# Optimization experiments

Hardware: AMD Instinct MI355X
Metric: run time of the kernel (lower is better)

## Reference

```python
import jax, jax.numpy as jnp
import numpy as np

B, T, F = 8, 1024, 80
STACK, STRIDE = 4, 4          # encoder.embed.right_context+1, subsampling_rate
G, E, C = 4, 16, 8192         # num_codebooks, embedding_dim, num_embeddings
DENC = 512                    # encoder.output_size()
TS = (T - STACK) // STRIDE + 1
FREG = 0.01                   # features_regularization_weight
EPS = 1e-5


def setup_inputs() -> dict:
    key = jax.random.key(0)
    ks = jax.random.split(key, 12)
    feats = jax.random.normal(ks[0], (B, T, F), jnp.float32)
    feats_lengths = jax.random.randint(ks[1], (B,), T // 2, T + 1, jnp.int32)
    # span masks (True = masked), mask_length=10 spans so full subsample windows get masked
    n_spans, ML = 16, 10
    starts = jax.random.randint(ks[2], (B, n_spans), 0, T - ML)
    pos = starts[:, :, None] + jnp.arange(ML)  # [B, n_spans, ML]
    masks = jnp.zeros((B, T), bool).at[jnp.arange(B)[:, None, None], pos].set(True)
    mask_emb = 0.1 * jax.random.normal(ks[3], (1, 1, F), jnp.float32)
    signal_mean = 0.1 * jax.random.normal(ks[4], (F,), jnp.float32)
    signal_istd = jax.random.uniform(ks[5], (F,), jnp.float32, 0.5, 1.5)
    projection = jax.random.normal(ks[6], (STACK * F, G * E), jnp.float32) * np.sqrt(2.0 / (STACK * F + G * E))
    embeddings = jax.random.normal(ks[7], (C, G, E), jnp.float32)
    encoder_top_n_out = 0.02 * jax.random.normal(ks[8], (G, DENC, C), jnp.float32)
    encoder_top_n_out_bias = jnp.zeros((G, C), jnp.float32)
    encoder_out = jax.random.normal(ks[9], (B, TS, DENC), jnp.float32)
    return {"feats": feats, "feats_lengths": feats_lengths, "masks": masks,
            "mask_emb": mask_emb, "signal_mean": signal_mean, "signal_istd": signal_istd,
            "projection": projection, "embeddings": embeddings,
            "encoder_top_n_out": encoder_top_n_out,
            "encoder_top_n_out_bias": encoder_top_n_out_bias,
            "encoder_out": encoder_out}


def _quantize_codes(latent, codebook):
    # latent: [N, G*E] -> codes [N, G]; codebook: [C, G, E]
    lat = latent.reshape(latent.shape[0], G, E)
    dist = (jnp.sum(lat ** 2, -1, keepdims=True)
            - 2.0 * jnp.einsum('ngd,cgd->ngc', lat, codebook)
            + jnp.sum(codebook ** 2, -1).T[None])  # [N, G, C]
    return jnp.argmin(dist, axis=-1)


def reference(feats, feats_lengths, masks, mask_emb, signal_mean, signal_istd,
              projection, embeddings, encoder_top_n_out, encoder_top_n_out_bias,
              encoder_out):
    # global CMVN
    xs = (feats - signal_mean) * signal_istd  # [B, T, F]
    features_pen = jnp.mean(xs ** 2)
    # masked signal (fed to the delegated encoder in the original; encoder_out stands in)
    _masked_xs = jnp.where(masks[:, :, None], mask_emb, xs)
    # unfold windows
    widx = jnp.arange(TS)[:, None] * STRIDE + jnp.arange(STACK)  # [TS, STACK]
    code_ids_mask = jnp.all(masks[:, widx], axis=2)  # [B, TS] (torch.min over bool window)
    stacked = xs[:, widx].reshape(B, TS, STACK * F)  # _stack_features on unmasked input
    # LayerNorm (no affine)
    mu = jnp.mean(stacked, -1, keepdims=True)
    var = jnp.var(stacked, -1, keepdims=True)
    normed = (stacked - mu) / jnp.sqrt(var + EPS)
    proj = normed @ projection  # [B, TS, G*E]
    target = _quantize_codes(proj.reshape(B * TS, G * E), embeddings).reshape(B, TS, G)
    # encoder output mask after subsampling
    lens_sub = jnp.maximum((feats_lengths - STACK) // STRIDE + 1, 0)
    out_mask = jnp.arange(TS)[None, :] < lens_sub[:, None]
    m = (out_mask & code_ids_mask).astype(jnp.float32)  # [B, TS]
    # big matmul: [B,1,TS,DENC] x [1,G,DENC,C] + bias -> [B,G,TS,C]
    logits = jnp.einsum('btd,gdc->bgtc', encoder_out, encoder_top_n_out) \
             + encoder_top_n_out_bias[None, :, None, :]
    logp = jax.nn.log_softmax(logits, axis=-1).transpose(0, 2, 1, 3)  # [B, TS, G, C]
    per = -jnp.take_along_axis(logp, target[..., None], axis=-1)[..., 0]  # [B, TS, G]
    denom = jnp.sum(m) + 1e-5
    loss = jnp.sum(per * m[:, :, None]) / (denom * G) + FREG * features_pen
    num_codes = jnp.sum(m) * G
    corr = (jnp.argmax(logits, -1).transpose(0, 2, 1) == target)
    codes_acc = jnp.sum(corr * m[:, :, None]) / num_codes
    vals = (target * m[:, :, None].astype(target.dtype)).reshape(-1)
    uniq_num_codes = jnp.zeros((C,), bool).at[vals].set(True).sum()
    return (loss, codes_acc, features_pen, num_codes, uniq_num_codes)
```

## Files before the change

kernel.cpp:

```cpp
#include <hip/hip_runtime.h>
#include <hip/hip_bf16.h>
#include <math.h>
#include <stddef.h>

#define NB 8
#define NT 1024
#define NF 80
#define NSTACK 4
#define NSTRIDE 4
#define NG 4
#define NE 16
#define NC 8192
#define ND 512
#define NTS 256
#define NP (NB*NTS)
#define SFD (NSTACK*NF)
#define FREG 0.01f
#define LNEPS 1e-5f

#define TCC 1024
#define CPT 4
#define PCH 16
#define PB 16

#define ROWS_MAX 2176
#define ROWCH 144
#define MT 9
#define QCH 16
#define QY 16
#define CT 128
#define QS 8

typedef __attribute__((ext_vector_type(8))) short short8;
typedef __attribute__((ext_vector_type(4))) float f32x4;

struct Ws {
  float penSum;
  unsigned int nA;
  unsigned int maskIsInt;
  unsigned int pad1;
  unsigned long long amax[NP*NG];
  float sumExp[NP*NG];
  float tLogit[NP*NG];
  int   targets[NP*NG];
  int   activeList[NP];
  unsigned int bitmap[NC/32];
  unsigned long long aminS[NP*NG*QS];
  float lat[NP][64];
  unsigned short aHiT[(size_t)(ND/8)*ROWS_MAX*8];
  unsigned short aLoT[(size_t)(ND/8)*ROWS_MAX*8];
  float part_se[NG][ROWS_MAX][CT];
  unsigned long long part_mx[NG][ROWS_MAX][CT];
};

__device__ inline unsigned short bf16_rne(float x) {
  unsigned u = __float_as_uint(x);
  unsigned r = u + 0x7FFFu + ((u >> 16) & 1u);
  return (unsigned short)(r >> 16);
}
__device__ inline unsigned fkey_asc(float d) {
  unsigned u = __float_as_uint(d);
  return (u & 0x80000000u) ? ~u : (u | 0x80000000u);
}

__global__ __launch_bounds__(256) void k_prologue(
    const float* __restrict__ feats, const float* __restrict__ mean,
    const float* __restrict__ istd, const unsigned char* __restrict__ m8,
    const int* __restrict__ lens, int doClear, Ws* ws) {
  const int tid = threadIdx.x;
  if (doClear) ws->aminS[(size_t)blockIdx.x*256 + tid] = ~0ull;

  const int N4 = NB*NT*NF/4;
  float s = 0.f;
  for (int i = blockIdx.x*256 + tid; i < N4; i += gridDim.x*256) {
    float4 v = reinterpret_cast<const float4*>(feats)[i];
    int f0 = (i*4) % NF;
    float x0 = (v.x - mean[f0+0]) * istd[f0+0];
    float x1 = (v.y - mean[f0+1]) * istd[f0+1];
    float x2 = (v.z - mean[f0+2]) * istd[f0+2];
    float x3 = (v.w - mean[f0+3]) * istd[f0+3];
    s += x0*x0 + x1*x1 + x2*x2 + x3*x3;
  }
  for (int o = 32; o; o >>= 1) s += __shfl_down(s, o);
  __shared__ float pr[4];
  if ((tid & 63) == 0) pr[tid >> 6] = s;
  __syncthreads();
  if (tid == 0) atomicAdd(&ws->penSum, pr[0]+pr[1]+pr[2]+pr[3]);

  if (blockIdx.x < NP/256) {
    __shared__ unsigned flag;
    if (tid == 0) flag = 0;
    __syncthreads();
    unsigned nz = 0;
    int base = tid * 32;
    for (int i = base; i < base + 32; ++i)
      if ((i & 3) && m8[i]) nz = 1;
    if (nz) atomicOr(&flag, 1u);
    __syncthreads();
    bool isInt = (flag == 0);

    int p = blockIdx.x*256 + tid;
    int b = p >> 8, ts = p & (NTS-1);
    int t0 = b*NT + ts*NSTRIDE;
    bool allm;
    if (isInt) {
      const int* m32 = (const int*)m8;
      allm = m32[t0] && m32[t0+1] && m32[t0+2] && m32[t0+3];
    } else {
      allm = m8[t0] && m8[t0+1] && m8[t0+2] && m8[t0+3];
    }
    int ls = (lens[b] - NSTACK)/NSTRIDE + 1;
    if (ls < 0) ls = 0;
    if (allm && ts < ls) {
      unsigned idx = atomicAdd(&ws->nA, 1u);
      ws->activeList[idx] = p;
    }
  }
}

__global__ __launch_bounds__(256) void k_latprep(
    const float* __restrict__ feats, const float* __restrict__ mean,
    const float* __restrict__ istd, const float* __restrict__ projw,
    const float* __restrict__ enc, Ws* ws) {
  int nA = (int)ws->nA;
  int ai = blockIdx.x;
  int limit = ((nA + ROWCH - 1) / ROWCH) * ROWCH;
  int tid = threadIdx.x;

  if (ai >= nA) {
    if (ai < limit && tid < 64) {
      short8 z;
      #pragma unroll
      for (int j = 0; j < 8; ++j) z[j] = 0;
      *reinterpret_cast<short8*>(ws->aHiT + ((size_t)tid*ROWS_MAX + ai)*8) = z;
      *reinterpret_cast<short8*>(ws->aLoT + ((size_t)tid*ROWS_MAX + ai)*8) = z;
    }
    return;
  }

  int p = ws->activeList[ai];
  if (tid < 64) {
    const float* src = enc + (size_t)p*ND + tid*8;
    float4 x0 = *reinterpret_cast<const float4*>(src);
    float4 x1 = *reinterpret_cast<const float4*>(src + 4);
    float xv[8] = {x0.x, x0.y, x0.z, x0.w, x1.x, x1.y, x1.z, x1.w};
    short8 h, l;
    #pragma unroll
    for (int j = 0; j < 8; ++j) {
      unsigned short hi = bf16_rne(xv[j]);
      float rem = xv[j] - __uint_as_float((unsigned)hi << 16);
      h[j] = (short)hi;
      l[j] = (short)bf16_rne(rem);
    }
    *reinterpret_cast<short8*>(ws->aHiT + ((size_t)tid*ROWS_MAX + ai)*8) = h;
    *reinterpret_cast<short8*>(ws->aLoT + ((size_t)tid*ROWS_MAX + ai)*8) = l;
  }

  int b = p >> 8, ts = p & (NTS-1);
  __shared__ float sN[SFD];
  __shared__ float sPart[4*64];
  __shared__ float rS[4], rQ[4];

  for (int j = tid; j < SFD; j += 256) {
    int k = j / NF, f = j - k*NF;
    sN[j] = (feats[((size_t)b*NT + ts*NSTRIDE + k)*NF + f] - mean[f]) * istd[f];
  }
  __syncthreads();
  float s = 0.f, q = 0.f;
  for (int j = tid; j < SFD; j += 256) { float x = sN[j]; s += x; q += x*x; }
  for (int o = 32; o; o >>= 1) { s += __shfl_down(s, o); q += __shfl_down(q, o); }
  if ((tid & 63) == 0) { rS[tid>>6] = s; rQ[tid>>6] = q; }
  __syncthreads();
  float mu  = (rS[0]+rS[1]+rS[2]+rS[3]) * (1.f/SFD);
  float var = (rQ[0]+rQ[1]+rQ[2]+rQ[3]) * (1.f/SFD) - mu*mu;
  float inv = rsqrtf(var + LNEPS);
  for (int j = tid; j < SFD; j += 256) sN[j] = (sN[j]-mu)*inv;
  __syncthreads();
  {
    int j = tid & 63, part = tid >> 6;
    float a = 0.f;
    int i0 = part*80;
    for (int i = i0; i < i0+80; ++i) a = fmaf(sN[i], projw[i*64 + j], a);
    sPart[part*64 + j] = a;
  }
  __syncthreads();
  if (tid < 64)
    ws->lat[ai][tid] = sPart[tid] + sPart[64+tid] + sPart[128+tid] + sPart[192+tid];
}

__global__ __launch_bounds__(256) void k_qdist(const float* __restrict__ emb, Ws* ws) {
  int nA = (int)ws->nA;
  if (nA == 0) return;
  int tid = threadIdx.x;
  int g = tid >> 6, lane = tid & 63;
  int c = blockIdx.x * 64 + lane;
  int per = (nA + QY - 1) / QY;
  int a0 = blockIdx.y * per;
  int a1 = min(nA, a0 + per);
  int slot = blockIdx.x & (QS-1);

  const float4* e4 = reinterpret_cast<const float4*>(emb + ((size_t)c*NG + g)*NE);
  float4 b0 = e4[0], b1 = e4[1], b2 = e4[2], b3 = e4[3];
  float n2 = b0.x*b0.x + b0.y*b0.y + b0.z*b0.z + b0.w*b0.w
           + b1.x*b1.x + b1.y*b1.y + b1.z*b1.z + b1.w*b1.w
           + b2.x*b2.x + b2.y*b2.y + b2.z*b2.z + b2.w*b2.w
           + b3.x*b3.x + b3.y*b3.y + b3.z*b3.z + b3.w*b3.w;

  __shared__ float sL[QCH][64];
  for (int base = a0; base < a1; base += QCH) {
    int cnt = min(QCH, a1 - base);
    __syncthreads();
    for (int i = tid; i < cnt*64; i += 256)
      (&sL[0][0])[i] = (&ws->lat[0][0])[(size_t)(base + (i >> 6))*64 + (i & 63)];
    __syncthreads();
    for (int i = 0; i < cnt; ++i) {
      const float* lp = &sL[i][g*NE];
      float dot = lp[0]*b0.x + lp[1]*b0.y + lp[2]*b0.z + lp[3]*b0.w
                + lp[4]*b1.x + lp[5]*b1.y + lp[6]*b1.z + lp[7]*b1.w
                + lp[8]*b2.x + lp[9]*b2.y + lp[10]*b2.z + lp[11]*b2.w
                + lp[12]*b3.x + lp[13]*b3.y + lp[14]*b3.z + lp[15]*b3.w;
      float d = n2 - 2.f*dot;
      float mv = d; int mc = c;
      #pragma unroll
      for (int off = 32; off; off >>= 1) {
        float ov = __shfl_xor(mv, off);
        int   oc = __shfl_xor(mc, off);
        if (ov < mv || (ov == mv && oc < mc)) { mv = ov; mc = oc; }
      }
      if (lane == 0) {
        unsigned long long key =
            ((unsigned long long)fkey_asc(mv) << 32) | (unsigned)mc;
        atomicMin(&ws->aminS[(size_t)((base + i)*NG + g)*QS + slot], key);
      }
    }
  }
}

__global__ void k_tgt(Ws* ws) {
  int i = blockIdx.x*256 + threadIdx.x;
  int nA = (int)ws->nA;
  if (i < nA*NG) {
    unsigned long long m = ws->aminS[(size_t)i*QS];
    #pragma unroll
    for (int s = 1; s < QS; ++s) {
      unsigned long long v = ws->aminS[(size_t)i*QS + s];
      if (v < m) m = v;
    }
    int c = (int)(unsigned)(m & 0xFFFFFFFFull);
    ws->targets[i] = c;
    atomicOr(&ws->bitmap[c >> 5], 1u << (c & 31));
  }
}

__global__ __launch_bounds__(512, 4) void k_logits_mfma(
    const float* __restrict__ W, const float* __restrict__ bias, Ws* ws) {
  const int nA = (int)ws->nA;
  if (nA == 0) return;
  const int nCh = (nA + ROWCH - 1) / ROWCH;
  const int tid = threadIdx.x;
  const int wave = tid >> 6, lane = tid & 63;
  const int sub = wave & 3, kh = wave >> 2;
  const int g = blockIdx.y;
  const int c0w = blockIdx.x * 64 + sub * 16;
  const int lo16 = lane & 15, hi4 = lane >> 4;
  const int cA = c0w + lo16;
  const int cOut0 = c0w + hi4*4;
  float bv[4];
  #pragma unroll
  for (int v = 0; v < 4; ++v) bv[v] = bias[g*NC + cOut0 + v];

  __shared__ f32x4 sAcc[4][MT][64];
  __shared__ float sEs[4][ROWCH];
  __shared__ unsigned long long sMx[4][ROWCH];

  for (int ch = 0; ch < nCh; ++ch) {
    const int r0 = ch * ROWCH;
    f32x4 acc[MT];
    #pragma unroll
    for (int mt = 0; mt < MT; ++mt) acc[mt] = (f32x4){0.f, 0.f, 0.f, 0.f};

    for (int ks = kh*8; ks < kh*8 + 8; ++ks) {
      short8 bh[MT], bl[MT];
      const size_t boff = ((size_t)(ks*4 + hi4)*ROWS_MAX + r0 + lo16)*8;
      #pragma unroll
      for (int mt = 0; mt < MT; ++mt) {
        bh[mt] = *reinterpret_cast<const short8*>(ws->aHiT + boff + (size_t)mt*128);
        bl[mt] = *reinterpret_cast<const short8*>(ws->aLoT + boff + (size_t)mt*128);
      }
      const float* wp = W + ((size_t)g*ND + ks*32 + hi4*8)*NC + cA;
      float wv[8];
      #pragma unroll
      for (int j = 0; j < 8; ++j) wv[j] = wp[(size_t)j*NC];
      short8 whi, wlo;
      #pragma unroll
      for (int j = 0; j < 8; ++j) {
        unsigned short h = bf16_rne(wv[j]);
        float rem = wv[j] - __uint_as_float((unsigned)h << 16);
        whi[j] = (short)h;
        wlo[j] = (short)bf16_rne(rem);
      }
      #pragma unroll
      for (int mt = 0; mt < MT; ++mt) {
        acc[mt] = __builtin_amdgcn_mfma_f32_16x16x32_bf16(whi, bh[mt], acc[mt], 0, 0, 0);
        acc[mt] = __builtin_amdgcn_mfma_f32_16x16x32_bf16(wlo, bh[mt], acc[mt], 0, 0, 0);
        acc[mt] = __builtin_amdgcn_mfma_f32_16x16x32_bf16(whi, bl[mt], acc[mt], 0, 0, 0);
      }
    }

    if (kh == 1) {
      #pragma unroll
      for (int mt = 0; mt < MT; ++mt) sAcc[sub][mt][lane] = acc[mt];
    }
    __syncthreads();

    if (kh == 0) {
      #pragma unroll
      for (int mt = 0; mt < MT; ++mt) {
        f32x4 oth = sAcc[sub][mt][lane];
        const int row = r0 + mt*16 + lo16;
        const int tgt = (row < nA) ? ws->targets[row*NG + g] : -1;
        float lv[4];
        #pragma unroll
        for (int v = 0; v < 4; ++v) lv[v] = (acc[mt][v] + oth[v]) + bv[v];
        #pragma unroll
        for (int v = 0; v < 4; ++v)
          if (tgt == cOut0 + v) ws->tLogit[row*NG + g] = lv[v];
        float es = expf(lv[0]) + expf(lv[1]) + expf(lv[2]) + expf(lv[3]);
        float mv = lv[0]; int mi = cOut0;
        if (lv[1] > mv) { mv = lv[1]; mi = cOut0+1; }
        if (lv[2] > mv) { mv = lv[2]; mi = cOut0+2; }
        if (lv[3] > mv) { mv = lv[3]; mi = cOut0+3; }
        #pragma unroll
        for (int off = 16; off <= 32; off <<= 1) {
          es += __shfl_xor(es, off);
          float ov = __shfl_xor(mv, off);
          int   oi = __shfl_xor(mi, off);
          if (ov > mv || (ov == mv && oi < mi)) { mv = ov; mi = oi; }
        }
        if (hi4 == 0) {
          sEs[sub][mt*16 + lo16] = es;
          unsigned key = __float_as_uint(mv);
          key = (key & 0x80000000u) ? ~key : (key | 0x80000000u);
          sMx[sub][mt*16 + lo16] = ((unsigned long long)key << 32)
                                 | (unsigned long long)(0xFFFFFFFFu - (unsigned)mi);
        }
      }
    }
    __syncthreads();
    if (tid < ROWCH) {
      float e = sEs[0][tid] + sEs[1][tid] + sEs[2][tid] + sEs[3][tid];
      unsigned long long m0 = sMx[0][tid], m1 = sMx[1][tid];
      unsigned long long m2 = sMx[2][tid], m3 = sMx[3][tid];
      unsigned long long ma = m0 > m1 ? m0 : m1;
      unsigned long long mb = m2 > m3 ? m2 : m3;
      unsigned long long mx = ma > mb ? ma : mb;
      int grow = r0 + tid;
      ws->part_se[g][grow][blockIdx.x] = e;
      ws->part_mx[g][grow][blockIdx.x] = mx;
    }
    __syncthreads();
  }
}

__global__ __launch_bounds__(256) void k_red_l(Ws* ws) {
  int nA = (int)ws->nA;
  int pair = blockIdx.x*4 + (threadIdx.x >> 6);
  int lane = threadIdx.x & 63;
  int row = pair >> 2, g = pair & 3;
  if (row >= nA) return;
  float e = ws->part_se[g][row][lane] + ws->part_se[g][row][lane + 64];
  unsigned long long a = ws->part_mx[g][row][lane];
  unsigned long long b = ws->part_mx[g][row][lane + 64];
  unsigned long long mx = a > b ? a : b;
  #pragma unroll
  for (int off = 32; off; off >>= 1) {
    e += __shfl_xor(e, off);
    unsigned long long o = __shfl_xor(mx, off);
    if (o > mx) mx = o;
  }
  if (lane == 0) {
    ws->sumExp[row*NG + g] = e;
    ws->amax[row*NG + g] = mx;
  }
}

__global__ __launch_bounds__(256) void k_quant(
    const float* __restrict__ feats, const float* __restrict__ mean,
    const float* __restrict__ istd, const float* __restrict__ projw,
    const float* __restrict__ emb, Ws* ws) {
  if (blockIdx.x >= ws->nA) return;
  int ai = blockIdx.x;
  int p = ws->activeList[ai];
  int b = p >> 8, ts = p & (NTS-1);
  int tid = threadIdx.x;
  __shared__ float sN[SFD];
  __shared__ float sPart[4*64];
  __shared__ float sLat[NG*NE];
  __shared__ float sRedS[256];
  __shared__ int   sRedC[256];
  __shared__ float rS[4], rQ[4];
  __shared__ int   sTgt[NG];

  for (int j = tid; j < SFD; j += 256) {
    int k = j / NF, f = j - k*NF;
    sN[j] = (feats[((size_t)b*NT + ts*NSTRIDE + k)*NF + f] - mean[f]) * istd[f];
  }
  __syncthreads();
  float s = 0.f, q = 0.f;
  for (int j = tid; j < SFD; j += 256) { float x = sN[j]; s += x; q += x*x; }
  for (int o = 32; o; o >>= 1) { s += __shfl_down(s, o); q += __shfl_down(q, o); }
  if ((tid & 63) == 0) { rS[tid>>6] = s; rQ[tid>>6] = q; }
  __syncthreads();
  float mu  = (rS[0]+rS[1]+rS[2]+rS[3]) * (1.f/SFD);
  float var = (rQ[0]+rQ[1]+rQ[2]+rQ[3]) * (1.f/SFD) - mu*mu;
  float inv = rsqrtf(var + LNEPS);
  for (int j = tid; j < SFD; j += 256) sN[j] = (sN[j]-mu)*inv;
  __syncthreads();
  {
    int j = tid & 63, part = tid >> 6;
    float a = 0.f;
    int i0 = part*80;
    for (int i = i0; i < i0+80; ++i) a = fmaf(sN[i], projw[i*64 + j], a);
    sPart[part*64 + j] = a;
  }
  __syncthreads();
  if (tid < 64) sLat[tid] = sPart[tid] + sPart[64+tid] + sPart[128+tid] + sPart[192+tid];
  __syncthreads();

  for (int gg = 0; gg < NG; ++gg) {
    float lg[NE];
    #pragma unroll
    for (int e = 0; e < NE; ++e) lg[e] = sLat[gg*NE + e];
    float best = 3.4e38f; int bc = NC;
    for (int c = tid; c < NC; c += 256) {
      const float4* cb4 = reinterpret_cast<const float4*>(emb + ((size_t)c*NG + gg)*NE);
      float4 a0 = cb4[0], a1 = cb4[1], a2 = cb4[2], a3 = cb4[3];
      float dot = 0.f, n2 = 0.f;
      dot = fmaf(lg[0],  a0.x, dot); n2 = fmaf(a0.x, a0.x, n2);
      dot = fmaf(lg[1],  a0.y, dot); n2 = fmaf(a0.y, a0.y, n2);
      dot = fmaf(lg[2],  a0.z, dot); n2 = fmaf(a0.z, a0.z, n2);
      dot = fmaf(lg[3],  a0.w, dot); n2 = fmaf(a0.w, a0.w, n2);
      dot = fmaf(lg[4],  a1.x, dot); n2 = fmaf(a1.x, a1.x, n2);
      dot = fmaf(lg[5],  a1.y, dot); n2 = fmaf(a1.y, a1.y, n2);
      dot = fmaf(lg[6],  a1.z, dot); n2 = fmaf(a1.z, a1.z, n2);
      dot = fmaf(lg[7],  a1.w, dot); n2 = fmaf(a1.w, a1.w, n2);
      dot = fmaf(lg[8],  a2.x, dot); n2 = fmaf(a2.x, a2.x, n2);
      dot = fmaf(lg[9],  a2.y, dot); n2 = fmaf(a2.y, a2.y, n2);
      dot = fmaf(lg[10], a2.z, dot); n2 = fmaf(a2.z, a2.z, n2);
      dot = fmaf(lg[11], a2.w, dot); n2 = fmaf(a2.w, a2.w, n2);
      dot = fmaf(lg[12], a3.x, dot); n2 = fmaf(a3.x, a3.x, n2);
      dot = fmaf(lg[13], a3.y, dot); n2 = fmaf(a3.y, a3.y, n2);
      dot = fmaf(lg[14], a3.z, dot); n2 = fmaf(a3.z, a3.z, n2);
      dot = fmaf(lg[15], a3.w, dot); n2 = fmaf(a3.w, a3.w, n2);
      float sc = n2 - 2.f*dot;
      if (sc < best) { best = sc; bc = c; }
    }
    sRedS[tid] = best; sRedC[tid] = bc;
    __syncthreads();
    for (int off = 128; off; off >>= 1) {
      if (tid < off) {
        float os = sRedS[tid+off]; int oc = sRedC[tid+off];
        if (os < sRedS[tid] || (os == sRedS[tid] && oc < sRedC[tid])) {
          sRedS[tid] = os; sRedC[tid] = oc;
        }
      }
      __syncthreads();
    }
    if (tid == 0) sTgt[gg] = sRedC[0];
    __syncthreads();
  }
  if (tid < NG) {
    int c = sTgt[tid];
    ws->targets[ai*NG + tid] = c;
    atomicOr(&ws->bitmap[c >> 5], 1u << (c & 31));
  }
}

__global__ __launch_bounds__(256) void k_logits(
    const float* __restrict__ W, const float* __restrict__ bias,
    const float* __restrict__ enc, Ws* ws) {
  const int nA = (int)ws->nA;
  if (nA == 0) return;
  const int nCh = (nA + PCH - 1) / PCH;
  const int g = blockIdx.y;
  const int cbase = blockIdx.x * TCC + threadIdx.x * CPT;
  const float* __restrict__ Wg = W + (size_t)g*ND*NC;
  const float b0 = bias[g*NC + cbase + 0];
  const float b1 = bias[g*NC + cbase + 1];
  const float b2 = bias[g*NC + cbase + 2];
  const float b3 = bias[g*NC + cbase + 3];
  __shared__ float4 sEnc[PCH][ND/4];
  __shared__ int sP[PCH];

  for (int ch = blockIdx.z; ch < nCh; ch += PB) {
    if (threadIdx.x < PCH) {
      int ai = ch*PCH + threadIdx.x;
      sP[threadIdx.x] = (ai < nA) ? ws->activeList[ai] : -1;
    }
    __syncthreads();
    for (int i = threadIdx.x; i < PCH*(ND/4); i += 256) {
      int qq = i >> 7, r = i & 127;
      int p = sP[qq];
      sEnc[qq][r] = (p >= 0) ? reinterpret_cast<const float4*>(enc)[p*(ND/4) + r]
                             : make_float4(0.f, 0.f, 0.f, 0.f);
    }
    __syncthreads();

    float acc[PCH][CPT];
    #pragma unroll
    for (int qq = 0; qq < PCH; ++qq)
      #pragma unroll
      for (int j = 0; j < CPT; ++j) acc[qq][j] = 0.f;
    for (int d = 0; d < ND; d += 4) {
      const float* wp = Wg + (size_t)d*NC + cbase;
      float4 w0 = *reinterpret_cast<const float4*>(wp);
      float4 w1 = *reinterpret_cast<const float4*>(wp + NC);
      float4 w2 = *reinterpret_cast<const float4*>(wp + 2*NC);
      float4 w3 = *reinterpret_cast<const float4*>(wp + 3*NC);
      int dq = d >> 2;
      #pragma unroll
      for (int qq = 0; qq < PCH; ++qq) {
        float4 e = sEnc[qq][dq];
        acc[qq][0] = fmaf(e.x, w0.x, acc[qq][0]);
        acc[qq][1] = fmaf(e.x, w0.y, acc[qq][1]);
        acc[qq][2] = fmaf(e.x, w0.z, acc[qq][2]);
        acc[qq][3] = fmaf(e.x, w0.w, acc[qq][3]);
        acc[qq][0] = fmaf(e.y, w1.x, acc[qq][0]);
        acc[qq][1] = fmaf(e.y, w1.y, acc[qq][1]);
        acc[qq][2] = fmaf(e.y, w1.z, acc[qq][2]);
        acc[qq][3] = fmaf(e.y, w1.w, acc[qq][3]);
        acc[qq][0] = fmaf(e.z, w2.x, acc[qq][0]);
        acc[qq][1] = fmaf(e.z, w2.y, acc[qq][1]);
        acc[qq][2] = fmaf(e.z, w2.z, acc[qq][2]);
        acc[qq][3] = fmaf(e.z, w2.w, acc[qq][3]);
        acc[qq][0] = fmaf(e.w, w3.x, acc[qq][0]);
        acc[qq][1] = fmaf(e.w, w3.y, acc[qq][1]);
        acc[qq][2] = fmaf(e.w, w3.z, acc[qq][2]);
        acc[qq][3] = fmaf(e.w, w3.w, acc[qq][3]);
      }
    }

    #pragma unroll
    for (int qq = 0; qq < PCH; ++qq) {
      int ai = ch*PCH + qq;
      if (ai < nA) {
        float l0 = acc[qq][0] + b0;
        float l1 = acc[qq][1] + b1;
        float l2 = acc[qq][2] + b2;
        float l3 = acc[qq][3] + b3;
        int tgt = ws->targets[ai*NG + g];
        if ((unsigned)(tgt - cbase) < (unsigned)CPT) {
          float tv = (tgt == cbase) ? l0 : (tgt == cbase+1) ? l1
                   : (tgt == cbase+2) ? l2 : l3;
          ws->tLogit[ai*NG + g] = tv;
        }
        float es = expf(l0) + expf(l1) + expf(l2) + expf(l3);
        float mv = l0; int mi = cbase;
        if (l1 > mv) { mv = l1; mi = cbase+1; }
        if (l2 > mv) { mv = l2; mi = cbase+2; }
        if (l3 > mv) { mv = l3; mi = cbase+3; }
        for (int o = 32; o; o >>= 1) {
          es += __shfl_down(es, o);
          float ov = __shfl_down(mv, o);
          int   oi = __shfl_down(mi, o);
          if (ov > mv || (ov == mv && oi < mi)) { mv = ov; mi = oi; }
        }
        if ((threadIdx.x & 63) == 0) {
          atomicAdd(&ws->sumExp[ai*NG + g], es);
          unsigned key = __float_as_uint(mv);
          key = (key & 0x80000000u) ? ~key : (key | 0x80000000u);
          unsigned long long pk =
              ((unsigned long long)key << 32) |
              (unsigned long long)(0xFFFFFFFFu - (unsigned)mi);
          atomicMax(&ws->amax[ai*NG + g], pk);
        }
      }
    }
    __syncthreads();
  }
}

__global__ __launch_bounds__(256) void k_final(Ws* ws, float* __restrict__ out) {
  int tid = threadIdx.x;
  int nA = (int)ws->nA;
  float sumPer = 0.f, sumCorr = 0.f;
  for (int i = tid; i < nA*NG; i += 256) {
    sumPer += logf(ws->sumExp[i]) - ws->tLogit[i];
    unsigned long long pk = ws->amax[i];
    int mi = (int)(0xFFFFFFFFu - (unsigned)(pk & 0xFFFFFFFFull));
    if (mi == ws->targets[i]) sumCorr += 1.f;
  }
  unsigned w = ws->bitmap[tid];
  if (tid == 0 && nA < NP) w |= 1u;
  int uniq = __popc(w);

  __shared__ float rs[4], rc[4]; __shared__ int ru[4];
  float s1 = sumPer, s2 = sumCorr; int s3 = uniq;
  for (int o = 32; o; o >>= 1) {
    s1 += __shfl_down(s1, o);
    s2 += __shfl_down(s2, o);
    s3 += __shfl_down(s3, o);
  }
  if ((tid & 63) == 0) { rs[tid>>6] = s1; rc[tid>>6] = s2; ru[tid>>6] = s3; }
  __syncthreads();
  if (tid == 0) {
    float sp = rs[0]+rs[1]+rs[2]+rs[3];
    float sc = rc[0]+rc[1]+rc[2]+rc[3];
    int   un = ru[0]+ru[1]+ru[2]+ru[3];
    float pen   = ws->penSum / (float)(NB*NT*NF);
    float denom = (float)nA + 1e-5f;
    float nc    = (float)(nA * NG);
    out[0] = sp / (denom * (float)NG) + FREG * pen;
    out[1] = sc / nc;
    out[2] = pen;
    out[3] = nc;
    out[4] = (float)un;
  }
}

extern "C" void kernel_launch(void* const* d_in, const int* in_sizes, int n_in,
                              void* d_out, int out_size, void* d_ws, size_t ws_size,
                              hipStream_t stream) {
  const float* feats = (const float*)d_in[0];
  const int*   lens  = (const int*)d_in[1];
  const unsigned char* masks = (const unsigned char*)d_in[2];
  const float* mean  = (const float*)d_in[4];
  const float* istd  = (const float*)d_in[5];
  const float* projw = (const float*)d_in[6];
  const float* emb   = (const float*)d_in[7];
  const float* W     = (const float*)d_in[8];
  const float* bias  = (const float*)d_in[9];
  const float* enc   = (const float*)d_in[10];
  Ws* ws = (Ws*)d_ws;
  float* out = (float*)d_out;

  bool big = ws_size >= sizeof(Ws);
  size_t zr = offsetof(Ws, aminS);
  hipMemsetAsync(d_ws, 0, (big || ws_size >= zr) ? zr : ws_size, stream);

  k_prologue<<<256, 256, 0, stream>>>(feats, mean, istd, masks, lens,
                                      big ? 1 : 0, ws);

  if (big) {
    k_latprep<<<ROWS_MAX, 256, 0, stream>>>(feats, mean, istd, projw, enc, ws);
    k_qdist<<<dim3(NC/64, QY), 256, 0, stream>>>(emb, ws);
    k_tgt<<<NP*NG/256, 256, 0, stream>>>(ws);
    k_logits_mfma<<<dim3(CT, NG), 512, 0, stream>>>(W, bias, ws);
    k_red_l<<<NP, 256, 0, stream>>>(ws);
  } else {
    k_quant<<<NP, 256, 0, stream>>>(feats, mean, istd, projw, emb, ws);
    k_logits<<<dim3(NC/TCC, NG, PB), 256, 0, stream>>>(W, bias, enc, ws);
  }
  k_final<<<1, 256, 0, stream>>>(ws, out);
}
```

Baseline: 83.30 us.

## Stage activation tiles in LDS with double-buffered async loads in logits MFMA

The logits kernel drops the split-K wave arrangement, so all 8 waves now cover distinct 16-column slices (128 columns per block instead of 64). The bf16 hi/lo activation tiles are staged into shared memory with global_load_lds and double-buffered across the K steps, and W values are prefetched one step ahead. This is meant to let the waves share activation loads instead of each re-reading them from global memory, and to remove the cross-wave partial-accumulator reduction. In exchange it adds a barrier per K step and more LDS use, and it halves the column-tile count (CT 64), so the launch has fewer blocks and k_red_l reduces 64 partials instead of 128.

```diff
diff --git a/kernel.cpp b/kernel.cpp
--- a/kernel.cpp
+++ b/kernel.cpp
@@ -28,8 +28,9 @@
 #define MT 9
 #define QCH 16
 #define QY 16
-#define CT 128
+#define CT 64
 #define QS 8
+#define STG 1152
 
 typedef __attribute__((ext_vector_type(8))) short short8;
 typedef __attribute__((ext_vector_type(4))) float f32x4;
@@ -62,6 +63,11 @@
   unsigned u = __float_as_uint(d);
   return (u & 0x80000000u) ? ~u : (u | 0x80000000u);
 }
+__device__ __forceinline__ void gload_lds16(const void* g, void* l) {
+  __builtin_amdgcn_global_load_lds(
+      (const __attribute__((address_space(1))) void*)g,
+      (__attribute__((address_space(3))) void*)l, 16, 0, 0);
+}
 
 __global__ __launch_bounds__(256) void k_prologue(
     const float* __restrict__ feats, const float* __restrict__ mean,
@@ -259,9 +265,9 @@
   const int nCh = (nA + ROWCH - 1) / ROWCH;
   const int tid = threadIdx.x;
   const int wave = tid >> 6, lane = tid & 63;
-  const int sub = wave & 3, kh = wave >> 2;
+  const int sub = wave;
   const int g = blockIdx.y;
-  const int c0w = blockIdx.x * 64 + sub * 16;
+  const int c0w = blockIdx.x * 128 + sub * 16;
   const int lo16 = lane & 15, hi4 = lane >> 4;
   const int cA = c0w + lo16;
   const int cOut0 = c0w + hi4*4;
@@ -269,28 +275,62 @@
   #pragma unroll
   for (int v = 0; v < 4; ++v) bv[v] = bias[g*NC + cOut0 + v];
 
-  __shared__ f32x4 sAcc[4][MT][64];
-  __shared__ float sEs[4][ROWCH];
-  __shared__ unsigned long long sMx[4][ROWCH];
+  __shared__ unsigned short sB[2*STG*8];
+  __shared__ float sEs[8][ROWCH];
+  __shared__ unsigned long long sMx[8][ROWCH];
+
+  const unsigned short* gB[3];
+  #pragma unroll
+  for (int it = 0; it < 3; ++it) {
+    int t = tid + it*512;
+    if (t < STG) {
+      int hilo = t / 576;
+      int r = t - hilo*576;
+      int h4 = r / 144;
+      int row = r - h4*144;
+      gB[it] = (hilo ? ws->aLoT : ws->aHiT) + ((size_t)h4*ROWS_MAX + row)*8;
+    }
+  }
 
   for (int ch = 0; ch < nCh; ++ch) {
     const int r0 = ch * ROWCH;
+    const size_t chOff = (size_t)r0*8;
+
+    #pragma unroll
+    for (int it = 0; it < 3; ++it) {
+      int t = tid + it*512;
+      if (t < STG)
+        gload_lds16(gB[it] + chOff, sB + (size_t)t*8);
+    }
+    float wv[8];
+    {
+      const float* wp = W + ((size_t)g*ND + hi4*8)*NC + cA;
+      #pragma unroll
+      for (int j = 0; j < 8; ++j) wv[j] = wp[(size_t)j*NC];
+    }
     f32x4 acc[MT];
     #pragma unroll
     for (int mt = 0; mt < MT; ++mt) acc[mt] = (f32x4){0.f, 0.f, 0.f, 0.f};
-
-    for (int ks = kh*8; ks < kh*8 + 8; ++ks) {
-      short8 bh[MT], bl[MT];
-      const size_t boff = ((size_t)(ks*4 + hi4)*ROWS_MAX + r0 + lo16)*8;
-      #pragma unroll
-      for (int mt = 0; mt < MT; ++mt) {
-        bh[mt] = *reinterpret_cast<const short8*>(ws->aHiT + boff + (size_t)mt*128);
-        bl[mt] = *reinterpret_cast<const short8*>(ws->aLoT + boff + (size_t)mt*128);
-      }
-      const float* wp = W + ((size_t)g*ND + ks*32 + hi4*8)*NC + cA;
-      float wv[8];
-      #pragma unroll
-      for (int j = 0; j < 8; ++j) wv[j] = wp[(size_t)j*NC];
+    __syncthreads();
+
+    #pragma unroll
+    for (int ks = 0; ks < ND/32; ++ks) {
+      const int cur = ks & 1;
+      if (ks < ND/32 - 1) {
+        const size_t ksOff = ((size_t)(ks+1)*4*ROWS_MAX)*8 + chOff;
+        #pragma unroll
+        for (int it = 0; it < 3; ++it) {
+          int t = tid + it*512;
+          if (t < STG)
+            gload_lds16(gB[it] + ksOff, sB + (size_t)(cur^1)*STG*8 + (size_t)t*8);
+        }
+      }
+      float wvn[8];
+      if (ks < ND/32 - 1) {
+        const float* wpn = W + ((size_t)g*ND + (ks+1)*32 + hi4*8)*NC + cA;
+        #pragma unroll
+        for (int j = 0; j < 8; ++j) wvn[j] = wpn[(size_t)j*NC];
+      }
       short8 whi, wlo;
       #pragma unroll
       for (int j = 0; j < 8; ++j) {
@@ -299,61 +339,63 @@
         whi[j] = (short)h;
         wlo[j] = (short)bf16_rne(rem);
       }
+      const unsigned short* bp0 =
+          sB + ((size_t)cur*STG + (size_t)hi4*144 + lo16)*8;
       #pragma unroll
       for (int mt = 0; mt < MT; ++mt) {
-        acc[mt] = __builtin_amdgcn_mfma_f32_16x16x32_bf16(whi, bh[mt], acc[mt], 0, 0, 0);
-        acc[mt] = __builtin_amdgcn_mfma_f32_16x16x32_bf16(wlo, bh[mt], acc[mt], 0, 0, 0);
-        acc[mt] = __builtin_amdgcn_mfma_f32_16x16x32_bf16(whi, bl[mt], acc[mt], 0, 0, 0);
-      }
-    }
-
-    if (kh == 1) {
-      #pragma unroll
-      for (int mt = 0; mt < MT; ++mt) sAcc[sub][mt][lane] = acc[mt];
-    }
-    __syncthreads();
-
-    if (kh == 0) {
-      #pragma unroll
-      for (int mt = 0; mt < MT; ++mt) {
-        f32x4 oth = sAcc[sub][mt][lane];
-        const int row = r0 + mt*16 + lo16;
-        const int tgt = (row < nA) ? ws->targets[row*NG + g] : -1;
-        float lv[4];
+        short8 bh = *reinterpret_cast<const short8*>(bp0 + (size_t)mt*128);
+        short8 bl = *reinterpret_cast<const short8*>(bp0 + 576*8 + (size_t)mt*128);
+        acc[mt] = __builtin_amdgcn_mfma_f32_16x16x32_bf16(whi, bh, acc[mt], 0, 0, 0);
+        acc[mt] = __builtin_amdgcn_mfma_f32_16x16x32_bf16(wlo, bh, acc[mt], 0, 0, 0);
+        acc[mt] = __builtin_amdgcn_mfma_f32_16x16x32_bf16(whi, bl, acc[mt], 0, 0, 0);
+      }
+      __syncthreads();
+      if (ks < ND/32 - 1) {
         #pragma unroll
-        for (int v = 0; v < 4; ++v) lv[v] = (acc[mt][v] + oth[v]) + bv[v];
-        #pragma unroll
-        for (int v = 0; v < 4; ++v)
-          if (tgt == cOut0 + v) ws->tLogit[row*NG + g] = lv[v];
-        float es = expf(lv[0]) + expf(lv[1]) + expf(lv[2]) + expf(lv[3]);
-        float mv = lv[0]; int mi = cOut0;
-        if (lv[1] > mv) { mv = lv[1]; mi = cOut0+1; }
-        if (lv[2] > mv) { mv = lv[2]; mi = cOut0+2; }
-        if (lv[3] > mv) { mv = lv[3]; mi = cOut0+3; }
-        #pragma unroll
-        for (int off = 16; off <= 32; off <<= 1) {
-          es += __shfl_xor(es, off);
-          float ov = __shfl_xor(mv, off);
-          int   oi = __shfl_xor(mi, off);
-          if (ov > mv || (ov == mv && oi < mi)) { mv = ov; mi = oi; }
-        }
-        if (hi4 == 0) {
-          sEs[sub][mt*16 + lo16] = es;
-          unsigned key = __float_as_uint(mv);
-          key = (key & 0x80000000u) ? ~key : (key | 0x80000000u);
-          sMx[sub][mt*16 + lo16] = ((unsigned long long)key << 32)
-                                 | (unsigned long long)(0xFFFFFFFFu - (unsigned)mi);
-        }
+        for (int j = 0; j < 8; ++j) wv[j] = wvn[j];
+      }
+    }
+
+    #pragma unroll
+    for (int mt = 0; mt < MT; ++mt) {
+      const int row = r0 + mt*16 + lo16;
+      const int tgt = (row < nA) ? ws->targets[row*NG + g] : -1;
+      float lv[4];
+      #pragma unroll
+      for (int v = 0; v < 4; ++v) lv[v] = acc[mt][v] + bv[v];
+      #pragma unroll
+      for (int v = 0; v < 4; ++v)
+        if (tgt == cOut0 + v) ws->tLogit[row*NG + g] = lv[v];
+      float es = expf(lv[0]) + expf(lv[1]) + expf(lv[2]) + expf(lv[3]);
+      float mv = lv[0]; int mi = cOut0;
+      if (lv[1] > mv) { mv = lv[1]; mi = cOut0+1; }
+      if (lv[2] > mv) { mv = lv[2]; mi = cOut0+2; }
+      if (lv[3] > mv) { mv = lv[3]; mi = cOut0+3; }
+      #pragma unroll
+      for (int off = 16; off <= 32; off <<= 1) {
+        es += __shfl_xor(es, off);
+        float ov = __shfl_xor(mv, off);
+        int   oi = __shfl_xor(mi, off);
+        if (ov > mv || (ov == mv && oi < mi)) { mv = ov; mi = oi; }
+      }
+      if (hi4 == 0) {
+        sEs[sub][mt*16 + lo16] = es;
+        unsigned key = __float_as_uint(mv);
+        key = (key & 0x80000000u) ? ~key : (key | 0x80000000u);
+        sMx[sub][mt*16 + lo16] = ((unsigned long long)key << 32)
+                               | (unsigned long long)(0xFFFFFFFFu - (unsigned)mi);
       }
     }
     __syncthreads();
     if (tid < ROWCH) {
-      float e = sEs[0][tid] + sEs[1][tid] + sEs[2][tid] + sEs[3][tid];
-      unsigned long long m0 = sMx[0][tid], m1 = sMx[1][tid];
-      unsigned long long m2 = sMx[2][tid], m3 = sMx[3][tid];
-      unsigned long long ma = m0 > m1 ? m0 : m1;
-      unsigned long long mb = m2 > m3 ? m2 : m3;
-      unsigned long long mx = ma > mb ? ma : mb;
+      float e = 0.f;
+      unsigned long long mx = 0;
+      #pragma unroll
+      for (int sbi = 0; sbi < 8; ++sbi) {
+        e += sEs[sbi][tid];
+        unsigned long long m = sMx[sbi][tid];
+        if (m > mx) mx = m;
+      }
       int grow = r0 + tid;
       ws->part_se[g][grow][blockIdx.x] = e;
       ws->part_mx[g][grow][blockIdx.x] = mx;
@@ -368,10 +410,8 @@
   int lane = threadIdx.x & 63;
   int row = pair >> 2, g = pair & 3;
   if (row >= nA) return;
-  float e = ws->part_se[g][row][lane] + ws->part_se[g][row][lane + 64];
-  unsigned long long a = ws->part_mx[g][row][lane];
-  unsigned long long b = ws->part_mx[g][row][lane + 64];
-  unsigned long long mx = a > b ? a : b;
+  float e = ws->part_se[g][row][lane];
+  unsigned long long mx = ws->part_mx[g][row][lane];
   #pragma unroll
   for (int off = 32; off; off >>= 1) {
     e += __shfl_xor(e, off);
```

After: 99.43 us. 19.4% more time.
